# Performance work log

Hardware: AMD Instinct MI355X
Metric: run time of the kernel (lower is better)

Reference implementation:

```python
import jax, jax.numpy as jnp
import numpy as np

DIM = 1024


def setup_inputs() -> dict:
    key = jax.random.key(0)
    ks = jax.random.split(key, 10)
    B, S, D = 4, 2048, DIM
    std = 1.0 / np.sqrt(D)  # torch Linear default uniform bound
    return {
        "query": jax.random.normal(ks[0], (B, S, D), jnp.float32),
        "key": jax.random.normal(ks[1], (B, S, D), jnp.float32),
        "value": jax.random.normal(ks[2], (B, S, D), jnp.float32),
        "context": jnp.zeros((D,), jnp.float32),
        "Wq": jax.random.uniform(ks[3], (D, D), jnp.float32, -std, std),
        "bq": jax.random.uniform(ks[4], (D,), jnp.float32, -std, std),
        "Wk": jax.random.uniform(ks[5], (D, D), jnp.float32, -std, std),
        "bk": jax.random.uniform(ks[6], (D,), jnp.float32, -std, std),
        "Wv": jax.random.uniform(ks[7], (D, D), jnp.float32, -std, std),
        "bv": jax.random.uniform(ks[8], (D,), jnp.float32, -std, std),
    }


def reference(query, key, value, context, Wq, bq, Wk, bk, Wv, bv):
    scale = query.shape[-1] ** -0.5
    # torch Linear: x @ W.T + b
    q = (query + context) @ Wq.T + bq          # [B,S,D]
    k = (key + context) @ Wk.T + bk            # [B,S,D]
    v = value @ Wv.T + bv                      # [B,S,D]
    scores = jnp.einsum("bqd,bkd->bqk", q, k) * scale  # [B,S,S]
    weights = jax.nn.softmax(scores, axis=-1)
    return jnp.einsum("bqk,bkd->bqd", weights, v)
```

## Files before the change

### kernel.cpp

```cpp
#include <hip/hip_runtime.h>

typedef __attribute__((ext_vector_type(8))) short bf16x8;
typedef __attribute__((ext_vector_type(4))) float floatx4;

constexpr int BATCH = 4;
constexpr int SEQ   = 2048;
constexpr int DIMN  = 1024;
constexpr int M1    = BATCH * SEQ;

__device__ __forceinline__ short f2bf(float f) {
    union { float f; unsigned u; } x; x.f = f;
    unsigned r = x.u + 0x7fffu + ((x.u >> 16) & 1u);
    return (short)(r >> 16);
}
__device__ __forceinline__ float bf2f(short s) {
    union { unsigned u; float f; } x; x.u = ((unsigned)(unsigned short)s) << 16;
    return x.f;
}

__device__ __forceinline__ void async16(const void* g, void* l) {
    __builtin_amdgcn_global_load_lds(
        (const __attribute__((address_space(1))) unsigned int*)g,
        (__attribute__((address_space(3))) unsigned int*)l, 16, 0, 0);
}

#define WAITVM(N) asm volatile("s_waitcnt vmcnt(" #N ")" ::: "memory")
#define MEMFENCE  asm volatile("" ::: "memory")
#define BAR()     __builtin_amdgcn_s_barrier()
#define PRIO(x)   __builtin_amdgcn_s_setprio(x)

template<bool OUT_BF16>
__device__ __forceinline__ void gemm256(
    const short* __restrict__ Ab, int lda,
    const short* __restrict__ Bb, int ldb,
    void* __restrict__ Cb, int ldc,
    const float* __restrict__ bias, int K, float scale,
    int m0, int n0)
{
    constexpr int ABY  = 32768;
    constexpr int BUFB = 65536;
    __shared__ alignas(16) char smem[2 * BUFB];
    char* lds = smem;

    const int t    = threadIdx.x;
    const int lane = t & 63;
    const int wave = t >> 6;
    const int wr   = wave >> 2;
    const int wc   = wave & 3;
    const int lr   = lane & 15;
    const int lq   = lane >> 4;

    const int srow  = t >> 3;
    const int scol  = (((t & 7) * 16) ^ ((srow & 7) << 4)) >> 1;
    const short* pa0 = Ab + (size_t)(m0 + srow) * lda + scol;
    const short* pb0 = Bb + (size_t)(n0 + srow) * ldb + scol;
    const size_t rsa = (size_t)64 * lda;
    const size_t rsb = (size_t)64 * ldb;
    const int ldst = t * 16;

    const int roA = (wr * 128 + lr) * 128;
    const int roB = ABY + (wc * 64 + lr) * 128;
    const int cs  = (lane & 7) << 4;
    const int cp0 = (lq << 4) ^ cs;
    const int cp1 = (64 | (lq << 4)) ^ cs;

    floatx4 acc[8][4];
    #pragma unroll
    for (int m = 0; m < 8; ++m)
        #pragma unroll
        for (int n = 0; n < 4; ++n) acc[m][n] = (floatx4)(0.f);

    auto stB01 = [&](int d, int kt) { const short* p = pb0 + kt * 64;
        async16(p,       lds + d + ABY +        ldst);
        async16(p + rsb, lds + d + ABY + 8192 + ldst); };
    auto stB23 = [&](int d, int kt) { const short* p = pb0 + kt * 64;
        async16(p + 2 * rsb, lds + d + ABY + 16384 + ldst);
        async16(p + 3 * rsb, lds + d + ABY + 24576 + ldst); };
    auto stA02 = [&](int d, int kt) { const short* p = pa0 + kt * 64;
        async16(p,           lds + d +         ldst);
        async16(p + 2 * rsa, lds + d + 16384 + ldst); };
    auto stA13 = [&](int d, int kt) { const short* p = pa0 + kt * 64;
        async16(p + rsa,     lds + d +  8192 + ldst);
        async16(p + 3 * rsa, lds + d + 24576 + ldst); };

    const int NT = K >> 6;

    stB01(0, 0); stB23(0, 0); stA02(0, 0); stA13(0, 0);
    if (NT > 1) { stB01(BUFB, 1); WAITVM(2); }
    else        { WAITVM(0); }
    BAR(); MEMFENCE;

    int bu = 0;
    for (int tt = 0; tt < NT; ++tt) {
        const int ob = bu ^ BUFB;
        const char* rb = lds + bu;
        bf16x8 a0[4], a1[4], bf4[4];

        #pragma unroll
        for (int m = 0; m < 4; ++m) a0[m]  = *(const bf16x8*)(rb + roA + m * 2048 + cp0);
        #pragma unroll
        for (int n = 0; n < 4; ++n) bf4[n] = *(const bf16x8*)(rb + roB + n * 2048 + cp0);
        if (tt + 1 < NT) stB23(ob, tt + 1);
        BAR(); MEMFENCE;
        PRIO(1);
        #pragma unroll
        for (int m = 0; m < 4; ++m)
            #pragma unroll
            for (int n = 0; n < 4; ++n)
                acc[m][n] = __builtin_amdgcn_mfma_f32_16x16x32_bf16(a0[m], bf4[n], acc[m][n], 0, 0, 0);
        PRIO(0); MEMFENCE;
        if (tt + 1 < NT) { WAITVM(4); } else { WAITVM(0); }
        BAR(); MEMFENCE;

        #pragma unroll
        for (int m = 0; m < 4; ++m) a1[m] = *(const bf16x8*)(rb + roA + (m + 4) * 2048 + cp0);
        if (tt + 1 < NT) stA02(ob, tt + 1);
        BAR(); MEMFENCE;
        PRIO(1);
        #pragma unroll
        for (int m = 0; m < 4; ++m)
            #pragma unroll
            for (int n = 0; n < 4; ++n)
                acc[m + 4][n] = __builtin_amdgcn_mfma_f32_16x16x32_bf16(a1[m], bf4[n], acc[m + 4][n], 0, 0, 0);
        PRIO(0); MEMFENCE;
        BAR(); MEMFENCE;

        #pragma unroll
        for (int m = 0; m < 4; ++m) a0[m]  = *(const bf16x8*)(rb + roA + m * 2048 + cp1);
        #pragma unroll
        for (int n = 0; n < 4; ++n) bf4[n] = *(const bf16x8*)(rb + roB + n * 2048 + cp1);
        if (tt + 1 < NT) stA13(ob, tt + 1);
        BAR(); MEMFENCE;
        PRIO(1);
        #pragma unroll
        for (int m = 0; m < 4; ++m)
            #pragma unroll
            for (int n = 0; n < 4; ++n)
                acc[m][n] = __builtin_amdgcn_mfma_f32_16x16x32_bf16(a0[m], bf4[n], acc[m][n], 0, 0, 0);
        PRIO(0); MEMFENCE;
        BAR(); MEMFENCE;

        #pragma unroll
        for (int m = 0; m < 4; ++m) a1[m] = *(const bf16x8*)(rb + roA + (m + 4) * 2048 + cp1);
        if (tt + 2 < NT) stB01(bu, tt + 2);
        BAR(); MEMFENCE;
        PRIO(1);
        #pragma unroll
        for (int m = 0; m < 4; ++m)
            #pragma unroll
            for (int n = 0; n < 4; ++n)
                acc[m + 4][n] = __builtin_amdgcn_mfma_f32_16x16x32_bf16(a1[m], bf4[n], acc[m + 4][n], 0, 0, 0);
        PRIO(0); MEMFENCE;
        if (tt + 1 < NT) {
            if (tt + 2 < NT) { WAITVM(4); } else { WAITVM(2); }
        }
        BAR(); MEMFENCE;
        bu = ob;
    }

    #pragma unroll
    for (int n = 0; n < 4; ++n) {
        const int gn = n0 + wc * 64 + n * 16 + lr;
        const float bv = bias ? bias[gn] : 0.f;
        #pragma unroll
        for (int m = 0; m < 8; ++m) {
            #pragma unroll
            for (int r = 0; r < 4; ++r) {
                const int gm = m0 + wr * 128 + m * 16 + lq * 4 + r;
                const float v = acc[m][n][r] * scale + bv;
                if (OUT_BF16) ((short*)Cb)[(size_t)gm * ldc + gn] = f2bf(v);
                else          ((float*)Cb)[(size_t)gm * ldc + gn] = v;
            }
        }
    }
}

template<bool OUT_BF16>
__device__ __forceinline__ void gemm128(
    const short* __restrict__ Ab, int lda,
    const short* __restrict__ Bb, int ldb,
    void* __restrict__ Cb, int ldc,
    const float* __restrict__ bias, int K, float scale,
    int m0, int n0)
{
    constexpr int ABY  = 16384;
    constexpr int BUFB = ABY + 32768;
    __shared__ alignas(16) char smem[3 * BUFB];
    char* lds = smem;

    const int t    = threadIdx.x;
    const int lane = t & 63;
    const int wave = t >> 6;
    const int wr   = wave >> 2;
    const int wc   = wave & 3;
    const int lr   = lane & 15;
    const int lq   = lane >> 4;

    const int srow  = t >> 3;
    const int scol  = (((t & 7) * 16) ^ ((srow & 7) << 4)) >> 1;
    const short* pa0 = Ab + (size_t)(m0 + srow) * lda + scol;
    const short* pb0 = Bb + (size_t)(n0 + srow) * ldb + scol;
    const size_t rsa = (size_t)64 * lda;
    const size_t rsb = (size_t)64 * ldb;
    const int ldst = t * 16;

    const int roA = (wr * 64 + lr) * 128;
    const int roB = ABY + (wc * 64 + lr) * 128;
    const int cs  = (lane & 7) << 4;
    const int cp0 = (lq << 4) ^ cs;
    const int cp1 = (64 | (lq << 4)) ^ cs;

    floatx4 acc[4][4];
    #pragma unroll
    for (int m = 0; m < 4; ++m)
        #pragma unroll
        for (int n = 0; n < 4; ++n) acc[m][n] = (floatx4)(0.f);

    auto stA = [&](int d, int kt) { const short* p = pa0 + kt * 64;
        async16(p,       lds + d +        ldst);
        async16(p + rsa, lds + d + 8192 + ldst); };
    auto stB01 = [&](int d, int kt) { const short* p = pb0 + kt * 64;
        async16(p,       lds + d + ABY +        ldst);
        async16(p + rsb, lds + d + ABY + 8192 + ldst); };
    auto stB23 = [&](int d, int kt) { const short* p = pb0 + kt * 64;
        async16(p + 2 * rsb, lds + d + ABY + 16384 + ldst);
        async16(p + 3 * rsb, lds + d + ABY + 24576 + ldst); };

    const int NT = K >> 6;

    stA(0, 0); stB01(0, 0); stB23(0, 0);
    if (NT > 1) { stA(BUFB, 1); stB01(BUFB, 1); stB23(BUFB, 1); WAITVM(6); }
    else        { WAITVM(0); }
    BAR(); MEMFENCE;

    int cb = 0;
    for (int tt = 0; tt < NT; ++tt) {
        const char* rb = lds + cb;
        int sb = cb + 2 * BUFB; if (sb >= 3 * BUFB) sb -= 3 * BUFB;
        bf16x8 a[4], b[4];

        #pragma unroll
        for (int m = 0; m < 4; ++m) a[m] = *(const bf16x8*)(rb + roA + m * 2048 + cp0);
        #pragma unroll
        for (int n = 0; n < 4; ++n) b[n] = *(const bf16x8*)(rb + roB + n * 2048 + cp0);
        if (tt + 2 < NT) { stA(sb, tt + 2); stB01(sb, tt + 2); }
        BAR(); MEMFENCE;
        PRIO(1);
        #pragma unroll
        for (int m = 0; m < 4; ++m)
            #pragma unroll
            for (int n = 0; n < 4; ++n)
                acc[m][n] = __builtin_amdgcn_mfma_f32_16x16x32_bf16(a[m], b[n], acc[m][n], 0, 0, 0);
        PRIO(0); MEMFENCE;
        BAR(); MEMFENCE;

        #pragma unroll
        for (int m = 0; m < 4; ++m) a[m] = *(const bf16x8*)(rb + roA + m * 2048 + cp1);
        #pragma unroll
        for (int n = 0; n < 4; ++n) b[n] = *(const bf16x8*)(rb + roB + n * 2048 + cp1);
        if (tt + 2 < NT) stB23(sb, tt + 2);
        BAR(); MEMFENCE;
        PRIO(1);
        #pragma unroll
        for (int m = 0; m < 4; ++m)
            #pragma unroll
            for (int n = 0; n < 4; ++n)
                acc[m][n] = __builtin_amdgcn_mfma_f32_16x16x32_bf16(a[m], b[n], acc[m][n], 0, 0, 0);
        PRIO(0); MEMFENCE;
        if (tt + 1 < NT) {
            if (tt + 2 < NT) { WAITVM(6); } else { WAITVM(0); }
        }
        BAR(); MEMFENCE;
        cb += BUFB; if (cb >= 3 * BUFB) cb = 0;
    }

    #pragma unroll
    for (int n = 0; n < 4; ++n) {
        const int gn = n0 + wc * 64 + n * 16 + lr;
        const float bv = bias ? bias[gn] : 0.f;
        #pragma unroll
        for (int m = 0; m < 4; ++m) {
            #pragma unroll
            for (int r = 0; r < 4; ++r) {
                const int gm = m0 + wr * 64 + m * 16 + lq * 4 + r;
                const float v = acc[m][n][r] * scale + bv;
                if (OUT_BF16) ((short*)Cb)[(size_t)gm * ldc + gn] = f2bf(v);
                else          ((float*)Cb)[(size_t)gm * ldc + gn] = v;
            }
        }
    }
}

__global__ __launch_bounds__(512, 2)
void proj_qkv(const short* __restrict__ xq, const short* __restrict__ xk,
              const short* __restrict__ xv,
              const short* __restrict__ Wq_, const short* __restrict__ Wk_,
              const short* __restrict__ Wv_,
              const float* __restrict__ bq_, const float* __restrict__ bk_,
              const float* __restrict__ bv_,
              short* __restrict__ q, short* __restrict__ k, short* __restrict__ vp)
{
    const int b   = blockIdx.x;
    const int xcd = b & 7;
    const int i   = b >> 3;
    const int z   = i >> 5;
    const int r   = i & 31;
    const int mm  = r >> 2;
    const int nn  = r & 3;
    const short* X = (z == 0) ? xq : (z == 1) ? xk : xv;
    const short* W = (z == 0) ? Wq_ : (z == 1) ? Wk_ : Wv_;
    const float* bb = (z == 0) ? bq_ : (z == 1) ? bk_ : bv_;
    short* O = (z == 0) ? q : (z == 1) ? k : vp;
    gemm128<true>(X, DIMN, W, DIMN, (void*)O, DIMN, bb, DIMN, 1.f,
                  (xcd * 8 + mm) * 128, nn * 256);
}

__global__ __launch_bounds__(512, 2)
void gemm_scores(const short* __restrict__ q, const short* __restrict__ k,
                 short* __restrict__ S, float scale)
{
    const int b   = blockIdx.x;
    const int xcd = b & 7;
    const int i   = b >> 3;
    const int bz  = xcd >> 1;
    const int mh  = xcd & 1;
    const int mm  = i >> 3;
    const int nn  = i & 7;
    gemm256<true>(q + (size_t)bz * SEQ * DIMN, DIMN,
                  k + (size_t)bz * SEQ * DIMN, DIMN,
                  (void*)(S + (size_t)bz * SEQ * SEQ), SEQ,
                  nullptr, DIMN, scale,
                  (mh * 4 + mm) * 256, nn * 256);
}

__global__ __launch_bounds__(512, 2)
void gemm_pv(const short* __restrict__ P, const short* __restrict__ vt,
             float* __restrict__ O)
{
    const int b   = blockIdx.x;
    const int xcd = b & 7;
    const int i   = b >> 3;
    const int bz  = xcd >> 1;
    const int mh  = xcd & 1;
    const int mm  = i >> 2;
    const int nn  = i & 3;
    gemm128<false>(P  + (size_t)bz * SEQ * SEQ,  SEQ,
                   vt + (size_t)bz * DIMN * SEQ, SEQ,
                   (void*)(O + (size_t)bz * SEQ * DIMN), DIMN,
                   nullptr, SEQ, 1.f,
                   (mh * 8 + mm) * 128, nn * 256);
}

__global__ __launch_bounds__(256)
void cvt_tri(const float* __restrict__ in0, short* __restrict__ out0,
             const float* __restrict__ in1, short* __restrict__ out1,
             const float* __restrict__ in2, short* __restrict__ out2, int n8)
{
    const int z = blockIdx.z;
    const float* in = (z == 0) ? in0 : (z == 1) ? in1 : in2;
    short* out      = (z == 0) ? out0 : (z == 1) ? out1 : out2;
    const int i = blockIdx.x * 256 + threadIdx.x;
    if (i >= n8) return;
    const float4 a0 = ((const float4*)in)[(size_t)i * 2];
    const float4 a1 = ((const float4*)in)[(size_t)i * 2 + 1];
    const float v[8] = {a0.x, a0.y, a0.z, a0.w, a1.x, a1.y, a1.z, a1.w};
    bf16x8 o;
    #pragma unroll
    for (int j = 0; j < 8; ++j) o[j] = f2bf(v[j]);
    *(bf16x8*)(out + (size_t)i * 8) = o;
}

__global__ __launch_bounds__(256)
void bias3(const float* __restrict__ Wq, const float* __restrict__ Wk,
           const float* __restrict__ Wv,
           const float* __restrict__ bq, const float* __restrict__ bk,
           const float* __restrict__ bv,
           const float* __restrict__ ctx,
           float* __restrict__ oq, float* __restrict__ ok, float* __restrict__ ov)
{
    const int z = blockIdx.y;
    const float* W = (z == 0) ? Wq : (z == 1) ? Wk : Wv;
    const float* b = (z == 0) ? bq : (z == 1) ? bk : bv;
    float*       o = (z == 0) ? oq : (z == 1) ? ok : ov;
    const int n    = blockIdx.x * 4 + (threadIdx.x >> 6);
    const int lane = threadIdx.x & 63;
    float s = 0.f;
    if (z < 2) {
        const float* row = W + (size_t)n * DIMN;
        for (int k = lane * 4; k < DIMN; k += 256) {
            const float4 x = *(const float4*)(row + k);
            const float4 c = *(const float4*)(ctx + k);
            s += x.x * c.x + x.y * c.y + x.z * c.z + x.w * c.w;
        }
        #pragma unroll
        for (int off = 32; off > 0; off >>= 1) s += __shfl_xor(s, off);
    }
    if (lane == 0) o[n] = b[n] + s;
}

__global__ __launch_bounds__(256)
void transpose_v(const short* __restrict__ in, short* __restrict__ out)
{
    __shared__ short t[64][68];
    const int b  = blockIdx.z;
    const int d0 = blockIdx.x * 64;
    const int s0 = blockIdx.y * 64;
    const int r  = threadIdx.x >> 3;
    const int c  = (threadIdx.x & 7) * 8;
    #pragma unroll
    for (int h = 0; h < 2; ++h) {
        const int s = r + h * 32;
        bf16x8 v = *(const bf16x8*)(in + ((size_t)b * SEQ + s0 + s) * DIMN + d0 + c);
        #pragma unroll
        for (int j = 0; j < 8; ++j) t[c + j][s] = v[j];
    }
    __syncthreads();
    #pragma unroll
    for (int h = 0; h < 2; ++h) {
        const int d = r + h * 32;
        bf16x8 v;
        #pragma unroll
        for (int j = 0; j < 8; ++j) v[j] = t[d][c + j];
        *(bf16x8*)(out + ((size_t)b * DIMN + d0 + d) * SEQ + s0 + c) = v;
    }
}

__global__ __launch_bounds__(256)
void softmax_kernel(short* __restrict__ P)
{
    const int bid = blockIdx.x;
    const int xcd = bid & 7;
    const int i   = bid >> 3;
    const int row = (xcd >> 1) * SEQ + (xcd & 1) * 1024 + i;
    short* p = P + (size_t)row * SEQ;
    const int t    = threadIdx.x;
    const int lane = t & 63;
    const int wave = t >> 6;
    __shared__ float red[8];

    bf16x8 raw = *(const bf16x8*)(p + t * 8);
    float v[8];
    float mx = -1e30f;
    #pragma unroll
    for (int j = 0; j < 8; ++j) { v[j] = bf2f(raw[j]); mx = fmaxf(mx, v[j]); }
    #pragma unroll
    for (int off = 32; off > 0; off >>= 1) mx = fmaxf(mx, __shfl_xor(mx, off));
    if (lane == 0) red[wave] = mx;
    __syncthreads();
    mx = fmaxf(fmaxf(red[0], red[1]), fmaxf(red[2], red[3]));

    float e[8], s = 0.f;
    #pragma unroll
    for (int j = 0; j < 8; ++j) { e[j] = __expf(v[j] - mx); s += e[j]; }
    #pragma unroll
    for (int off = 32; off > 0; off >>= 1) s += __shfl_xor(s, off);
    if (lane == 0) red[4 + wave] = s;
    __syncthreads();
    s = red[4] + red[5] + red[6] + red[7];
    const float inv = 1.f / s;

    bf16x8 o;
    #pragma unroll
    for (int j = 0; j < 8; ++j) o[j] = f2bf(e[j] * inv);
    *(bf16x8*)(p + t * 8) = o;
}

extern "C" void kernel_launch(void* const* d_in, const int* in_sizes, int n_in,
                              void* d_out, int out_size, void* d_ws, size_t ws_size,
                              hipStream_t stream)
{
    const float* query = (const float*)d_in[0];
    const float* key_  = (const float*)d_in[1];
    const float* value = (const float*)d_in[2];
    const float* ctx   = (const float*)d_in[3];
    const float* Wq    = (const float*)d_in[4];
    const float* bq    = (const float*)d_in[5];
    const float* Wk    = (const float*)d_in[6];
    const float* bk    = (const float*)d_in[7];
    const float* Wv    = (const float*)d_in[8];
    const float* bv    = (const float*)d_in[9];

    char* ws = (char*)d_ws;
    char* od = (char*)d_out;
    const size_t MB = 1ull << 20;
    short* xq   = (short*)(ws);
    short* xk   = (short*)(ws + 16 * MB);
    short* q_b  = (short*)(ws + 32 * MB);
    short* k_b  = (short*)(ws + 48 * MB);
    short* Wq_b = (short*)(ws + 64 * MB);
    short* Wk_b = (short*)(ws + 66 * MB);
    short* Wv_b = (short*)(ws + 68 * MB);
    float* bq_e = (float*)(ws + 70 * MB);
    float* bk_e = (float*)(ws + 70 * MB + 4096);
    float* bv_e = (float*)(ws + 70 * MB + 8192);
    short* S_b  = (short*)(ws);
    short* v_t  = (short*)(ws + 64 * MB);
    short* xv   = (short*)(od);
    short* vp   = (short*)(od + 16 * MB);

    dim3 blk(256);
    dim3 blk512(512);
    const int W8 = DIMN * DIMN / 8;
    const int X8 = M1 * DIMN / 8;

    cvt_tri<<<dim3(W8 / 256, 1, 3), blk, 0, stream>>>(Wq, Wq_b, Wk, Wk_b, Wv, Wv_b, W8);
    bias3<<<dim3(DIMN / 4, 3), blk, 0, stream>>>(Wq, Wk, Wv, bq, bk, bv, ctx,
                                                 bq_e, bk_e, bv_e);
    cvt_tri<<<dim3(X8 / 256, 1, 3), blk, 0, stream>>>(query, xq, key_, xk, value, xv, X8);

    proj_qkv<<<dim3(768), blk512, 0, stream>>>(xq, xk, xv, Wq_b, Wk_b, Wv_b,
                                               bq_e, bk_e, bv_e, q_b, k_b, vp);
    transpose_v<<<dim3(DIMN / 64, SEQ / 64, BATCH), blk, 0, stream>>>(vp, v_t);

    const float scale = 1.0f / 32.0f;
    gemm_scores<<<dim3(256), blk512, 0, stream>>>(q_b, k_b, S_b, scale);

    softmax_kernel<<<dim3(M1), blk, 0, stream>>>(S_b);

    gemm_pv<<<dim3(256), blk512, 0, stream>>>(S_b, v_t, (float*)d_out);
}
```

Baseline: 308.6 us.

## Use smaller 128x128 GEMM tiles for QKV projection and merge conversion launches

Adds a new 256-thread GEMM routine with 128x128 tiles and a 32-wide K step, and switches the QKV projection to it. The launch grows from 768 to 1536 blocks at four blocks per CU, aiming for better occupancy and load balance. The weight and activation bf16 conversions are merged into one six-slice launch to save a kernel launch. The cost is less data reuse per tile and more global traffic, since each K step stages less data. The merged launch also has many idle blocks in the weight slices, which return early.

```diff
diff --git a/kernel.cpp b/kernel.cpp
--- a/kernel.cpp
+++ b/kernel.cpp
@@ -28,6 +28,96 @@
 #define MEMFENCE  asm volatile("" ::: "memory")
 #define BAR()     __builtin_amdgcn_s_barrier()
 #define PRIO(x)   __builtin_amdgcn_s_setprio(x)
+
+template<bool OUT_BF16>
+__device__ __forceinline__ void gemm97(
+    const short* __restrict__ Ab, int lda,
+    const short* __restrict__ Bb, int ldb,
+    void* __restrict__ Cb, int ldc,
+    const float* __restrict__ bias, int K, float scale,
+    int m0, int n0)
+{
+    constexpr int ABY  = 8192;
+    constexpr int BUFB = 16384;
+    __shared__ alignas(16) char smem[2 * BUFB];
+    char* lds = smem;
+
+    const int t    = threadIdx.x;
+    const int lane = t & 63;
+    const int wave = t >> 6;
+    const int wr   = wave >> 1;
+    const int wc   = wave & 1;
+    const int lr   = lane & 15;
+    const int lq   = lane >> 4;
+
+    const int srow  = t >> 2;
+    const int scolb = ((t & 3) * 16) ^ ((srow & 6) << 3);
+    const short* pa = Ab + (size_t)(m0 + srow) * lda + (scolb >> 1);
+    const short* pb = Bb + (size_t)(n0 + srow) * ldb + (scolb >> 1);
+    const size_t rsa = (size_t)64 * lda;
+    const size_t rsb = (size_t)64 * ldb;
+    const int ldst = t * 16;
+
+    const int cp  = ((lq ^ ((lr >> 1) & 3)) << 4);
+    const int roA = (wr * 64 + lr) * 64;
+    const int roB = ABY + (wc * 64 + lr) * 64;
+
+    floatx4 acc[4][4];
+    #pragma unroll
+    for (int m = 0; m < 4; ++m)
+        #pragma unroll
+        for (int n = 0; n < 4; ++n) acc[m][n] = (floatx4)(0.f);
+
+    auto stage = [&](int d, int kt) {
+        const short* qa = pa + kt * 32;
+        const short* qb = pb + kt * 32;
+        async16(qa,       lds + d +        ldst);
+        async16(qa + rsa, lds + d + 4096 + ldst);
+        async16(qb,       lds + d + ABY +        ldst);
+        async16(qb + rsb, lds + d + ABY + 4096 + ldst);
+    };
+
+    const int NT = K >> 5;
+
+    stage(0, 0);
+    WAITVM(0);
+    BAR(); MEMFENCE;
+
+    for (int tt = 0; tt < NT; ++tt) {
+        const char* rb = lds + (tt & 1) * BUFB;
+        bf16x8 a[4], b[4];
+        #pragma unroll
+        for (int m = 0; m < 4; ++m) a[m] = *(const bf16x8*)(rb + roA + m * 1024 + cp);
+        #pragma unroll
+        for (int n = 0; n < 4; ++n) b[n] = *(const bf16x8*)(rb + roB + n * 1024 + cp);
+        if (tt + 1 < NT) stage(((tt + 1) & 1) * BUFB, tt + 1);
+        PRIO(1);
+        #pragma unroll
+        for (int m = 0; m < 4; ++m)
+            #pragma unroll
+            for (int n = 0; n < 4; ++n)
+                acc[m][n] = __builtin_amdgcn_mfma_f32_16x16x32_bf16(a[m], b[n], acc[m][n], 0, 0, 0);
+        PRIO(0); MEMFENCE;
+        if (tt + 1 < NT) WAITVM(0);
+        BAR(); MEMFENCE;
+    }
+
+    #pragma unroll
+    for (int n = 0; n < 4; ++n) {
+        const int gn = n0 + wc * 64 + n * 16 + lr;
+        const float bv = bias ? bias[gn] : 0.f;
+        #pragma unroll
+        for (int m = 0; m < 4; ++m) {
+            #pragma unroll
+            for (int r = 0; r < 4; ++r) {
+                const int gm = m0 + wr * 64 + m * 16 + lq * 4 + r;
+                const float v = acc[m][n][r] * scale + bv;
+                if (OUT_BF16) ((short*)Cb)[(size_t)gm * ldc + gn] = f2bf(v);
+                else          ((float*)Cb)[(size_t)gm * ldc + gn] = v;
+            }
+        }
+    }
+}
 
 template<bool OUT_BF16>
 __device__ __forceinline__ void gemm256(
@@ -291,7 +381,7 @@
     }
 }
 
-__global__ __launch_bounds__(512, 2)
+__global__ __launch_bounds__(256, 4)
 void proj_qkv(const short* __restrict__ xq, const short* __restrict__ xk,
               const short* __restrict__ xv,
               const short* __restrict__ Wq_, const short* __restrict__ Wk_,
@@ -303,16 +393,16 @@
     const int b   = blockIdx.x;
     const int xcd = b & 7;
     const int i   = b >> 3;
-    const int z   = i >> 5;
-    const int r   = i & 31;
-    const int mm  = r >> 2;
-    const int nn  = r & 3;
+    const int z   = i >> 6;
+    const int r   = i & 63;
+    const int mm  = r >> 3;
+    const int nn  = r & 7;
     const short* X = (z == 0) ? xq : (z == 1) ? xk : xv;
     const short* W = (z == 0) ? Wq_ : (z == 1) ? Wk_ : Wv_;
     const float* bb = (z == 0) ? bq_ : (z == 1) ? bk_ : bv_;
     short* O = (z == 0) ? q : (z == 1) ? k : vp;
-    gemm128<true>(X, DIMN, W, DIMN, (void*)O, DIMN, bb, DIMN, 1.f,
-                  (xcd * 8 + mm) * 128, nn * 256);
+    gemm97<true>(X, DIMN, W, DIMN, (void*)O, DIMN, bb, DIMN, 1.f,
+                 (xcd * 8 + mm) * 128, nn * 128);
 }
 
 __global__ __launch_bounds__(512, 2)
@@ -352,13 +442,24 @@
 }
 
 __global__ __launch_bounds__(256)
-void cvt_tri(const float* __restrict__ in0, short* __restrict__ out0,
-             const float* __restrict__ in1, short* __restrict__ out1,
-             const float* __restrict__ in2, short* __restrict__ out2, int n8)
+void cvt6(const float* __restrict__ w0, short* __restrict__ ow0,
+          const float* __restrict__ w1, short* __restrict__ ow1,
+          const float* __restrict__ w2, short* __restrict__ ow2,
+          const float* __restrict__ x0, short* __restrict__ ox0,
+          const float* __restrict__ x1, short* __restrict__ ox1,
+          const float* __restrict__ x2, short* __restrict__ ox2,
+          int n8w, int n8x)
 {
     const int z = blockIdx.z;
-    const float* in = (z == 0) ? in0 : (z == 1) ? in1 : in2;
-    short* out      = (z == 0) ? out0 : (z == 1) ? out1 : out2;
+    const float* in; short* out; int n8;
+    switch (z) {
+        case 0: in = w0; out = ow0; n8 = n8w; break;
+        case 1: in = w1; out = ow1; n8 = n8w; break;
+        case 2: in = w2; out = ow2; n8 = n8w; break;
+        case 3: in = x0; out = ox0; n8 = n8x; break;
+        case 4: in = x1; out = ox1; n8 = n8x; break;
+        default: in = x2; out = ox2; n8 = n8x; break;
+    }
     const int i = blockIdx.x * 256 + threadIdx.x;
     if (i >= n8) return;
     const float4 a0 = ((const float4*)in)[(size_t)i * 2];
@@ -503,13 +604,14 @@
     const int W8 = DIMN * DIMN / 8;
     const int X8 = M1 * DIMN / 8;
 
-    cvt_tri<<<dim3(W8 / 256, 1, 3), blk, 0, stream>>>(Wq, Wq_b, Wk, Wk_b, Wv, Wv_b, W8);
+    cvt6<<<dim3(X8 / 256, 1, 6), blk, 0, stream>>>(Wq, Wq_b, Wk, Wk_b, Wv, Wv_b,
+                                                   query, xq, key_, xk, value, xv,
+                                                   W8, X8);
     bias3<<<dim3(DIMN / 4, 3), blk, 0, stream>>>(Wq, Wk, Wv, bq, bk, bv, ctx,
                                                  bq_e, bk_e, bv_e);
-    cvt_tri<<<dim3(X8 / 256, 1, 3), blk, 0, stream>>>(query, xq, key_, xk, value, xv, X8);
-
-    proj_qkv<<<dim3(768), blk512, 0, stream>>>(xq, xk, xv, Wq_b, Wk_b, Wv_b,
-                                               bq_e, bk_e, bv_e, q_b, k_b, vp);
+
+    proj_qkv<<<dim3(1536), blk, 0, stream>>>(xq, xk, xv, Wq_b, Wk_b, Wv_b,
+                                             bq_e, bk_e, bv_e, q_b, k_b, vp);
     transpose_v<<<dim3(DIMN / 64, SEQ / 64, BATCH), blk, 0, stream>>>(vp, v_t);
 
     const float scale = 1.0f / 32.0f;
```

After: 319.2 us. 3.4% more time.
